# Kernel optimization log

Hardware: AMD Instinct MI355X
Metric: run time of the kernel (lower is better)

Reference implementation:

```python
import jax, jax.numpy as jnp
import numpy as np
import math

K = 8       # wavelet order (k)
C = 8       # channels (c)
ALPHA = 64  # retained Fourier modes
L = 0       # coarsest level
B = 32
N = 8192    # power of two


def setup_inputs() -> dict:
    key = jax.random.key(0)
    ks = jax.random.split(key, 14)
    ck = C * K
    scale = 1.0 / (ck * ck)  # matches torch: 1/(c*k)**2
    f32 = jnp.float32
    inp = {
        "x": jax.random.normal(ks[0], (B, N, C, K), dtype=f32),
        # SparseKernelFT1d weights (complex, stored as re/im): scale * rand
        "wA_re": scale * jax.random.uniform(ks[1], (ck, ck, ALPHA), dtype=f32),
        "wA_im": scale * jax.random.uniform(ks[2], (ck, ck, ALPHA), dtype=f32),
        "wB_re": scale * jax.random.uniform(ks[3], (ck, ck, ALPHA), dtype=f32),
        "wB_im": scale * jax.random.uniform(ks[4], (ck, ck, ALPHA), dtype=f32),
        "wC_re": scale * jax.random.uniform(ks[5], (ck, ck, ALPHA), dtype=f32),
        "wC_im": scale * jax.random.uniform(ks[6], (ck, ck, ALPHA), dtype=f32),
        # T0 linear layer (k -> k)
        "T0_w": jax.random.normal(ks[7], (K, K), dtype=f32) / math.sqrt(K),
        "T0_b": 0.01 * jax.random.normal(ks[8], (K,), dtype=f32),
        # Legendre wavelet filter buffers: ec_* are [H0.T;H1.T] / [G0.T;G1.T] (2k,k),
        # rc_* are [H0;G0] / [H1;G1] (2k,k). Stand-ins: random orthonormal-ish matrices
        # scaled like wavelet filters (same math regardless of exact values).
        "ec_s": jax.random.normal(ks[9], (2 * K, K), dtype=f32) / math.sqrt(2 * K),
        "ec_d": jax.random.normal(ks[10], (2 * K, K), dtype=f32) / math.sqrt(2 * K),
        "rc_e": jax.random.normal(ks[11], (2 * K, K), dtype=f32) / math.sqrt(2 * K),
        "rc_o": jax.random.normal(ks[12], (2 * K, K), dtype=f32) / math.sqrt(2 * K),
    }
    return inp


def _sparse_ft(x, w_re, w_im):
    # x: [B, N, c, k] -> spectral mixing over first ALPHA rfft modes
    Bb, Nn, c, k = x.shape
    xv = x.reshape(Bb, Nn, c * k).transpose(0, 2, 1)   # [B, ck, N]
    xf = jnp.fft.rfft(xv)                               # [B, ck, N//2+1] complex
    l = min(ALPHA, Nn // 2 + 1)
    W = (w_re[:, :, :l] + 1j * w_im[:, :, :l]).astype(jnp.complex64)
    of = jnp.einsum('bix,iox->box', xf[:, :, :l], W)
    out_ft = jnp.zeros((Bb, c * k, Nn // 2 + 1), dtype=jnp.complex64).at[:, :, :l].set(of)
    xo = jnp.fft.irfft(out_ft, n=Nn)                    # [B, ck, N] real
    return xo.transpose(0, 2, 1).reshape(Bb, Nn, c, k)


def reference(x, wA_re, wA_im, wB_re, wB_im, wC_re, wC_im, T0_w, T0_b,
              ec_s, ec_d, rc_e, rc_o):
    Bb, Nn, c, k = x.shape
    ns = int(math.floor(math.log2(Nn)))
    Ud, Us = [], []
    # --- decomposition ---
    for _ in range(ns - L):
        xa = jnp.concatenate([x[:, ::2], x[:, 1::2]], axis=-1)  # [B, N/2, c, 2k]
        d = xa @ ec_d                                           # [B, N/2, c, k]
        s = xa @ ec_s
        Ud.append(_sparse_ft(d, wA_re, wA_im) + _sparse_ft(s, wB_re, wB_im))
        Us.append(_sparse_ft(d, wC_re, wC_im))
        x = s
    # --- coarsest-level linear ---
    x = x @ T0_w.T + T0_b
    # --- reconstruction (u_s is None branch) ---
    for i in range(ns - 1 - L, -1, -1):
        x = x + Us[i]
        xc = jnp.concatenate([x, Ud[i]], axis=-1)               # [B, n, c, 2k]
        x_e = xc @ rc_e
        x_o = xc @ rc_o
        Bc, Nc, cc, _ = xc.shape
        x = jnp.stack([x_e, x_o], axis=2).reshape(Bc, Nc * 2, cc, K)  # interleave even/odd
    return (x,) + tuple(Ud) + tuple(Us)
```

## Files before the change

### kernel.cpp

```cpp
#include <hip/hip_runtime.h>

#define BB 32
#define CKD 64
#define CC 8
#define KK 8
#define TT 64
#define FPW 132

__device__ const int D_FCB[14] = {0,8,12,14,15,16,17,18,19,20,21,22,23,24};
__device__ const int D_TB[14] = {0,64,96,112,120,124,126,127,128,129,130,131,132,133};
__device__ const int D_LS[14] = {0,64,128,192,256,320,384,417,434,443,448,451,453,454};
__device__ const int D_L[13]  = {64,64,64,64,64,64,33,17,9,5,3,2,1};
__device__ const int D_FTOF[13] = {0,524288,786432,917504,983040,1015808,1032192,
                                   1048576,1064960,1081344,1097728,1114112,1130496};

typedef __attribute__((ext_vector_type(4))) short s4v;
typedef __attribute__((ext_vector_type(8))) short s8v;
typedef __attribute__((ext_vector_type(4))) float f4v;

static __device__ __forceinline__ float4 ld4(const float* p){ return *(const float4*)p; }
static __device__ __forceinline__ size_t d_udo(int i){ return 33554432ull - (16777216u >> i); }
static __device__ __forceinline__ size_t d_uso(int i){ return 50329600ull - (16777216u >> i); }
static __device__ __forceinline__ size_t d_tof(int i){ return 128ull * (8192u - (8192u >> i)); }

static __device__ __forceinline__ unsigned short b16(float f) {
    unsigned u = __float_as_uint(f);
    u += 0x7FFFu + ((u >> 16) & 1u);
    return (unsigned short)(u >> 16);
}
static __device__ __forceinline__ float fb16(unsigned short h) {
    return __uint_as_float(((unsigned)h) << 16);
}

__global__ __launch_bounds__(256) void gen_T_k(unsigned short* __restrict__ Th,
                                               unsigned short* __restrict__ Tl) {
    int lvl = blockIdx.y;
    int nh = 4096 >> lvl;
    int idx = blockIdx.x * 256 + threadIdx.x;
    if (idx >= nh * 128) return;
    int t = idx >> 7, k = idx & 127, x = k >> 1;
    int l = nh / 2 + 1; if (l > 64) l = 64;
    float v = 0.f;
    if (x < l) {
        int r = (x * t) & (nh - 1);
        float th = 6.283185307179586f * ((float)r / (float)nh);
        float s, c; sincosf(th, &s, &c);
        v = (k & 1) ? s : c;
    }
    unsigned short hi = b16(v);
    unsigned short lo = b16(v - fb16(hi));
    size_t off = d_tof(lvl) + idx;
    Th[off] = hi; Tl[off] = lo;
}

__global__ __launch_bounds__(256) void gen_Tf_k(unsigned short* __restrict__ Tfh,
                                                unsigned short* __restrict__ Tfl) {
    int lvl = blockIdx.y;
    int nh = 4096 >> lvl;
    int nhp = nh < 128 ? 128 : nh;
    int idx = blockIdx.x * 256 + threadIdx.x;
    if (idx >= 128 * nhp) return;
    int tb = 31 - __clz(nhp);
    int m = idx >> tb, t = idx & (nhp - 1);
    int x = m >> 1;
    int l = nh / 2 + 1; if (l > 64) l = 64;
    float v = 0.f;
    if (x < l && t < nh) {
        int r = (x * t) & (nh - 1);
        float th = 6.283185307179586f * ((float)r / (float)nh);
        float s, c; sincosf(th, &s, &c);
        v = (m & 1) ? -s : c;
    }
    unsigned short hi = b16(v);
    unsigned short lo = b16(v - fb16(hi));
    size_t off = (size_t)D_FTOF[lvl] + idx;
    Tfh[off] = hi; Tfl[off] = lo;
}

__global__ __launch_bounds__(256) void decomp_k(const float* __restrict__ xin,
        const float* __restrict__ ecd, const float* __restrict__ ecs,
        float* __restrict__ dslot, float* __restrict__ sslot, int nh) {
    int idx = blockIdx.x * 256 + threadIdx.x;
    if (idx >= BB * nh * CC) return;
    int c = idx & 7;
    int t = (idx >> 3) % nh;
    int b = idx / (nh * CC);
    const float* p0 = xin + ((size_t)b * 2 * nh + 2 * t) * CKD + c * KK;
    float xa[16];
    float4 v;
    v = ld4(p0);      xa[0]=v.x; xa[1]=v.y; xa[2]=v.z; xa[3]=v.w;
    v = ld4(p0+4);    xa[4]=v.x; xa[5]=v.y; xa[6]=v.z; xa[7]=v.w;
    v = ld4(p0+64);   xa[8]=v.x; xa[9]=v.y; xa[10]=v.z; xa[11]=v.w;
    v = ld4(p0+68);   xa[12]=v.x; xa[13]=v.y; xa[14]=v.z; xa[15]=v.w;
    float dd[8], ss[8];
    #pragma unroll
    for (int m = 0; m < 8; m++) { dd[m] = 0.f; ss[m] = 0.f; }
    #pragma unroll
    for (int j = 0; j < 16; j++) {
        float xv = xa[j];
        #pragma unroll
        for (int m = 0; m < 8; m++) {
            dd[m] = fmaf(xv, ecd[j*8+m], dd[m]);
            ss[m] = fmaf(xv, ecs[j*8+m], ss[m]);
        }
    }
    size_t ob = ((size_t)b * nh + t) * CKD + c * KK;
    *(float4*)(dslot+ob)   = make_float4(dd[0],dd[1],dd[2],dd[3]);
    *(float4*)(dslot+ob+4) = make_float4(dd[4],dd[5],dd[6],dd[7]);
    *(float4*)(sslot+ob)   = make_float4(ss[0],ss[1],ss[2],ss[3]);
    *(float4*)(sslot+ob+4) = make_float4(ss[4],ss[5],ss[6],ss[7]);
}

__global__ __launch_bounds__(256) void fft_fwd_mfma_k(const float* __restrict__ outbuf,
        const unsigned short* __restrict__ Tfh, const unsigned short* __restrict__ Tfl,
        float* __restrict__ xfpf) {
    __shared__ unsigned vp[64*FPW];
    int slot = blockIdx.x;
    int lvl = 0;
    while (lvl < 12 && slot >= D_FCB[lvl+1]) lvl++;
    int nh = 4096 >> lvl;
    int nhp = nh < 128 ? 128 : nh;
    int t0s = (slot - D_FCB[lvl]) * 512;
    int t1s = t0s + 512; if (t1s > nhp) t1s = nhp;
    int b = blockIdx.y, z = blockIdx.z;
    const float* V = outbuf + (z ? d_uso(lvl) : d_udo(lvl)) + (size_t)b * nh * CKD;
    const unsigned short* TH = Tfh + D_FTOF[lvl];
    const unsigned short* TL = Tfl + D_FTOF[lvl];
    int tid = threadIdx.x;
    int w = tid >> 6, lane = tid & 63;
    int col = lane & 15, khi = lane >> 4;
    int mt0 = (w & 1) * 4, nt0 = (w >> 1) * 2;
    f4v acc[4][2];
    #pragma unroll
    for (int m = 0; m < 4; m++)
        #pragma unroll
        for (int n = 0; n < 2; n++) acc[m][n] = (f4v){0.f,0.f,0.f,0.f};
    int rrow[2], rswz[2];
    #pragma unroll
    for (int n = 0; n < 2; n++) {
        rrow[n] = (nt0 + n)*16 + col;
        rswz[n] = ((rrow[n] >> 3) & 7) << 2;
    }
    for (int tc = t0s; tc < t1s; tc += 128) {
        __syncthreads();
        #pragma unroll
        for (int q = 0; q < 8; q++) {
            int fi = tid + 256*q;
            int t = tc + (fi >> 4);
            int i4 = (fi & 15) * 4;
            float4 v = make_float4(0.f,0.f,0.f,0.f);
            if (t < nh) v = ld4(V + (size_t)t*CKD + i4);
            int tl_ = t - tc;
            const float* pv = &v.x;
            #pragma unroll
            for (int j = 0; j < 4; j++) {
                int row = i4 + j;
                float f = pv[j];
                unsigned u = __float_as_uint(f);
                unsigned hi = u & 0xFFFF0000u;
                float r = f - __uint_as_float(hi);
                unsigned lo = __float_as_uint(r) & 0xFFFF0000u;
                int cw = tl_ ^ (((row >> 3) & 7) << 2);
                vp[row*FPW + cw] = (hi >> 16) | lo;
            }
        }
        __syncthreads();
        #pragma unroll
        for (int kk = 0; kk < 4; kk++) {
            int tg = tc + kk*32 + khi*8;
            s8v ah[4], al[4];
            #pragma unroll
            for (int m = 0; m < 4; m++) {
                int row = (mt0 + m)*16 + col;
                ah[m] = *(const s8v*)(TH + (size_t)row*nhp + tg);
                al[m] = *(const s8v*)(TL + (size_t)row*nhp + tg);
            }
            int cb = kk*32 + khi*8;
            #pragma unroll
            for (int n = 0; n < 2; n++) {
                const unsigned* pr = vp + rrow[n]*FPW;
                uint4 w0 = *(const uint4*)(pr + (cb ^ rswz[n]));
                uint4 w1 = *(const uint4*)(pr + ((cb + 4) ^ rswz[n]));
                s8v bh, bl;
                const unsigned* pw = &w0.x;
                #pragma unroll
                for (int j = 0; j < 4; j++) {
                    bh[j] = (short)(pw[j] & 0xFFFFu);
                    bl[j] = (short)(pw[j] >> 16);
                }
                pw = &w1.x;
                #pragma unroll
                for (int j = 0; j < 4; j++) {
                    bh[4+j] = (short)(pw[j] & 0xFFFFu);
                    bl[4+j] = (short)(pw[j] >> 16);
                }
                #pragma unroll
                for (int m = 0; m < 4; m++) {
                    acc[m][n] = __builtin_amdgcn_mfma_f32_16x16x32_bf16(ah[m], bh, acc[m][n], 0,0,0);
                    acc[m][n] = __builtin_amdgcn_mfma_f32_16x16x32_bf16(ah[m], bl, acc[m][n], 0,0,0);
                    acc[m][n] = __builtin_amdgcn_mfma_f32_16x16x32_bf16(al[m], bh, acc[m][n], 0,0,0);
                }
            }
        }
    }
    float* P = xfpf + ((size_t)slot*64 + (size_t)b*2 + z) * 8192;
    #pragma unroll
    for (int m = 0; m < 4; m++) {
        int m0 = (mt0 + m)*16 + khi*4;
        #pragma unroll
        for (int n = 0; n < 2; n++) {
            int ic = (nt0 + n)*16 + col;
            #pragma unroll
            for (int r = 0; r < 4; r++)
                P[(size_t)(m0 + r)*64 + ic] = acc[m][n][r];
        }
    }
}

__global__ __launch_bounds__(256) void reduce_fwd_k(const float* __restrict__ xfpf,
        float2* __restrict__ xf_all) {
    int lvl = blockIdx.y;
    int e = blockIdx.x * 256 + threadIdx.x;
    int j = e & 4095;
    int bz = e >> 12;
    int x = j >> 6, i = j & 63;
    int c0 = D_FCB[lvl], c1 = D_FCB[lvl+1];
    float re = 0.f, im = 0.f;
    for (int c = c0; c < c1; c++) {
        size_t base = ((size_t)c*64 + bz) * 8192;
        re += xfpf[base + (size_t)(2*x)*64 + i];
        im += xfpf[base + (size_t)(2*x+1)*64 + i];
    }
    xf_all[(size_t)lvl*262144 + (size_t)bz*4096 + j] = make_float2(re, im);
}

__global__ __launch_bounds__(256) void mix_all_k(const float2* __restrict__ xf_all,
        const float* __restrict__ wAr, const float* __restrict__ wAi,
        const float* __restrict__ wBr, const float* __restrict__ wBi,
        const float* __restrict__ wCr, const float* __restrict__ wCi,
        unsigned short* __restrict__ ofh, unsigned short* __restrict__ ofl) {
    int lvl = 0;
    while (lvl < 12 && (int)blockIdx.x >= D_LS[lvl+1]) lvl++;
    int x = blockIdx.x - D_LS[lvl];
    int nh = 4096 >> lvl;
    const float2* xfL = xf_all + (size_t)lvl*262144;
    int tid = threadIdx.x;
    int o = tid & 63, wq = tid >> 6;
    __shared__ float2 sxd[BB*CKD];
    __shared__ float2 sxs[BB*CKD];
    __shared__ float  swt[6][16*CKD];
    for (int q = tid; q < BB*CKD; q += 256) {
        int b = q >> 6, i = q & 63;
        sxd[q] = xfL[((size_t)b*2 + 0)*4096 + x*64 + i];
        sxs[q] = xfL[((size_t)b*2 + 1)*4096 + x*64 + i];
    }
    float2 aud[8], aus[8];
    #pragma unroll
    for (int j=0;j<8;j++){ aud[j]=make_float2(0.f,0.f); aus[j]=make_float2(0.f,0.f); }
    for (int ic = 0; ic < 4; ic++) {
        __syncthreads();
        for (int q = tid; q < 16*CKD; q += 256) {
            int ii = q >> 6, oo = q & 63;
            size_t a = ((size_t)(ic*16+ii)*64 + oo)*64 + x;
            swt[0][q] = wAr[a]; swt[1][q] = wAi[a];
            swt[2][q] = wBr[a]; swt[3][q] = wBi[a];
            swt[4][q] = wCr[a]; swt[5][q] = wCi[a];
        }
        __syncthreads();
        #pragma unroll 4
        for (int ii = 0; ii < 16; ii++) {
            float ar = swt[0][ii*64+o], ai_ = swt[1][ii*64+o];
            float br = swt[2][ii*64+o], bi_ = swt[3][ii*64+o];
            float cr = swt[4][ii*64+o], ci_ = swt[5][ii*64+o];
            int i = ic*16 + ii;
            #pragma unroll
            for (int j = 0; j < 8; j++) {
                float2 xd = sxd[(wq*8+j)*64 + i];
                float2 xs = sxs[(wq*8+j)*64 + i];
                aud[j].x += xd.x*ar - xd.y*ai_ + xs.x*br - xs.y*bi_;
                aud[j].y += xd.x*ai_ + xd.y*ar + xs.x*bi_ + xs.y*br;
                aus[j].x += xd.x*cr - xd.y*ci_;
                aus[j].y += xd.x*ci_ + xd.y*cr;
            }
        }
    }
    float w = (x == 0 || 2*x == nh) ? 1.f : 2.f;
    float sc = w / (float)nh;
    int k0 = 2*x;
    #pragma unroll
    for (int j = 0; j < 8; j++) {
        int b = wq*8 + j;
        {
            size_t base = (((size_t)lvl*32 + b)*2 + 0)*8192;
            float A = sc*aud[j].x, Bn = -sc*aud[j].y;
            unsigned short ha = b16(A),  hb = b16(Bn);
            unsigned short la = b16(A - fb16(ha)), lb = b16(Bn - fb16(hb));
            ofh[base + (size_t)k0*64 + o]     = ha;
            ofh[base + (size_t)(k0+1)*64 + o] = hb;
            ofl[base + (size_t)k0*64 + o]     = la;
            ofl[base + (size_t)(k0+1)*64 + o] = lb;
        }
        {
            size_t base = (((size_t)lvl*32 + b)*2 + 1)*8192;
            float A = sc*aus[j].x, Bn = -sc*aus[j].y;
            unsigned short ha = b16(A),  hb = b16(Bn);
            unsigned short la = b16(A - fb16(ha)), lb = b16(Bn - fb16(hb));
            ofh[base + (size_t)k0*64 + o]     = ha;
            ofh[base + (size_t)(k0+1)*64 + o] = hb;
            ofl[base + (size_t)k0*64 + o]     = la;
            ofl[base + (size_t)(k0+1)*64 + o] = lb;
        }
    }
}

__global__ __launch_bounds__(256) void fft_inv_mfma_k(
        const unsigned short* __restrict__ ofh, const unsigned short* __restrict__ ofl,
        const unsigned short* __restrict__ Th,  const unsigned short* __restrict__ Tl,
        float* __restrict__ outbuf) {
    __shared__ unsigned short gh[64*132];
    __shared__ unsigned short gl[64*132];
    int lvl = 0;
    while (lvl < 12 && (int)blockIdx.x >= D_TB[lvl+1]) lvl++;
    int g = blockIdx.x - D_TB[lvl];
    int nh = 4096 >> lvl;
    int tbase = g * 64;
    int b = blockIdx.y, z = blockIdx.z;
    const unsigned short* Gh = ofh + (((size_t)lvl*32 + b)*2 + z)*8192;
    const unsigned short* Gl = ofl + (((size_t)lvl*32 + b)*2 + z)*8192;
    int tid = threadIdx.x;
    #pragma unroll
    for (int q = 0; q < 4; q++) {
        int fi = tid + 256*q;
        int k = fi & 127, oct = fi >> 7;
        uint4 vh = *(const uint4*)(Gh + (size_t)k*64 + oct*8);
        uint4 vl = *(const uint4*)(Gl + (size_t)k*64 + oct*8);
        const unsigned* ph = &vh.x;
        const unsigned* pl = &vl.x;
        #pragma unroll
        for (int i = 0; i < 8; i++) {
            unsigned wd = ph[i>>1];
            gh[(oct*8+i)*132 + k] = (i&1) ? (unsigned short)(wd>>16) : (unsigned short)(wd&0xFFFF);
            wd = pl[i>>1];
            gl[(oct*8+i)*132 + k] = (i&1) ? (unsigned short)(wd>>16) : (unsigned short)(wd&0xFFFF);
        }
    }
    __syncthreads();
    int w = tid >> 6;
    int lane = tid & 63;
    int tb = tbase + w*16;
    if (tb >= nh) return;
    int trow = lane & 15, khi = lane >> 4;
    int tA = tb + trow; if (tA >= nh) tA = nh - 1;
    const unsigned short* THp = Th + d_tof(lvl) + (size_t)tA*128 + khi*8;
    const unsigned short* TLp = Tl + d_tof(lvl) + (size_t)tA*128 + khi*8;
    f4v acc[4];
    #pragma unroll
    for (int n = 0; n < 4; n++) acc[n] = (f4v){0.f,0.f,0.f,0.f};
    #pragma unroll
    for (int kk = 0; kk < 4; kk++) {
        s8v ah = *(const s8v*)(THp + kk*32);
        s8v al = *(const s8v*)(TLp + kk*32);
        #pragma unroll
        for (int n = 0; n < 4; n++) {
            int off = (n*16 + trow)*132 + kk*32 + khi*8;
            s4v b0 = *(const s4v*)(gh + off);
            s4v b1 = *(const s4v*)(gh + off + 4);
            s4v c0 = *(const s4v*)(gl + off);
            s4v c1 = *(const s4v*)(gl + off + 4);
            s8v bh = __builtin_shufflevector(b0, b1, 0,1,2,3,4,5,6,7);
            s8v bl = __builtin_shufflevector(c0, c1, 0,1,2,3,4,5,6,7);
            acc[n] = __builtin_amdgcn_mfma_f32_16x16x32_bf16(ah, bh, acc[n], 0, 0, 0);
            acc[n] = __builtin_amdgcn_mfma_f32_16x16x32_bf16(ah, bl, acc[n], 0, 0, 0);
            acc[n] = __builtin_amdgcn_mfma_f32_16x16x32_bf16(al, bh, acc[n], 0, 0, 0);
        }
    }
    float* U = outbuf + (z ? d_uso(lvl) : d_udo(lvl)) + (size_t)b * nh * CKD;
    int thi4 = (lane >> 4) * 4;
    #pragma unroll
    for (int n = 0; n < 4; n++) {
        #pragma unroll
        for (int r = 0; r < 4; r++) {
            int t = tb + thi4 + r;
            if (t < nh) U[(size_t)t*64 + n*16 + trow] = acc[n][r];
        }
    }
}

__global__ __launch_bounds__(256) void t0_k(const float* __restrict__ xin,
        const float* __restrict__ w, const float* __restrict__ bias,
        float* __restrict__ xout) {
    int idx = blockIdx.x*256 + threadIdx.x;
    if (idx >= BB*CKD) return;
    int m = idx & 7, c = (idx >> 3) & 7, b = idx >> 6;
    const float* xr = xin + (size_t)b*CKD + c*KK;
    float acc = bias[m];
    #pragma unroll
    for (int j = 0; j < 8; j++) acc = fmaf(xr[j], w[m*8+j], acc);
    xout[idx] = acc;
}

__global__ __launch_bounds__(256) void recon_k(const float* __restrict__ xin,
        const float* __restrict__ us, const float* __restrict__ ud,
        const float* __restrict__ rce, const float* __restrict__ rco,
        float* __restrict__ xout, int nh) {
    int idx = blockIdx.x*256 + threadIdx.x;
    if (idx >= BB*nh*CC) return;
    int c = idx & 7;
    int t = (idx >> 3) % nh;
    int b = idx / (nh*CC);
    size_t base = ((size_t)b*nh + t)*CKD + c*KK;
    float xc[16];
    float4 a0 = ld4(xin+base), a1 = ld4(xin+base+4);
    float4 u0 = ld4(us+base),  u1 = ld4(us+base+4);
    float4 d0 = ld4(ud+base),  d1 = ld4(ud+base+4);
    xc[0]=a0.x+u0.x; xc[1]=a0.y+u0.y; xc[2]=a0.z+u0.z; xc[3]=a0.w+u0.w;
    xc[4]=a1.x+u1.x; xc[5]=a1.y+u1.y; xc[6]=a1.z+u1.z; xc[7]=a1.w+u1.w;
    xc[8]=d0.x;  xc[9]=d0.y;  xc[10]=d0.z; xc[11]=d0.w;
    xc[12]=d1.x; xc[13]=d1.y; xc[14]=d1.z; xc[15]=d1.w;
    float e[8], o2[8];
    #pragma unroll
    for (int m = 0; m < 8; m++) { e[m] = 0.f; o2[m] = 0.f; }
    #pragma unroll
    for (int j = 0; j < 16; j++) {
        float xv = xc[j];
        #pragma unroll
        for (int m = 0; m < 8; m++) {
            e[m]  = fmaf(xv, rce[j*8+m], e[m]);
            o2[m] = fmaf(xv, rco[j*8+m], o2[m]);
        }
    }
    size_t ob = ((size_t)b*2*nh + 2*t)*CKD + c*KK;
    *(float4*)(xout+ob)      = make_float4(e[0],e[1],e[2],e[3]);
    *(float4*)(xout+ob+4)    = make_float4(e[4],e[5],e[6],e[7]);
    *(float4*)(xout+ob+64)   = make_float4(o2[0],o2[1],o2[2],o2[3]);
    *(float4*)(xout+ob+68)   = make_float4(o2[4],o2[5],o2[6],o2[7]);
}

extern "C" void kernel_launch(void* const* d_in, const int* in_sizes, int n_in,
                              void* d_out, int out_size, void* d_ws, size_t ws_size,
                              hipStream_t stream) {
    const float* x   = (const float*)d_in[0];
    const float* wAr = (const float*)d_in[1];
    const float* wAi = (const float*)d_in[2];
    const float* wBr = (const float*)d_in[3];
    const float* wBi = (const float*)d_in[4];
    const float* wCr = (const float*)d_in[5];
    const float* wCi = (const float*)d_in[6];
    const float* T0w = (const float*)d_in[7];
    const float* T0b = (const float*)d_in[8];
    const float* ecs = (const float*)d_in[9];
    const float* ecd = (const float*)d_in[10];
    const float* rce = (const float*)d_in[11];
    const float* rco = (const float*)d_in[12];
    float* out = (float*)d_out;
    float* wsf = (float*)d_ws;

    size_t p = 0;
    float2* xf_all = (float2*)(wsf + p); p += 6815744;
    unsigned short* ofh = (unsigned short*)(wsf + p); p += 3407872;
    unsigned short* ofl = (unsigned short*)(wsf + p); p += 3407872;
    unsigned short* Th  = (unsigned short*)(wsf + p); p += 528384;
    unsigned short* Tl  = (unsigned short*)(wsf + p); p += 528384;
    unsigned short* Tfh = (unsigned short*)(wsf + p); p += 573440;
    unsigned short* Tfl = (unsigned short*)(wsf + p); p += 573440;
    float*  xt0  = wsf + p; p += 2048;
    float*  rb0  = wsf + p; p += 4194304;
    float*  rb1  = wsf + p; p += 8388608;
    float*  xfpf = wsf + p; p += 12582912;
    (void)ws_size; (void)in_sizes; (void)n_in; (void)out_size;

    size_t udo[13], uso[13];
    for (int i = 0; i < 13; i++) {
        udo[i] = 33554432ull - (16777216u >> i);
        uso[i] = 50329600ull - (16777216u >> i);
    }

    gen_T_k<<<dim3(2048, 13), 256, 0, stream>>>(Th, Tl);
    gen_Tf_k<<<dim3(2048, 13), 256, 0, stream>>>(Tfh, Tfl);

    for (int i = 0; i < 13; i++) {
        int nh = 4096 >> i;
        const float* xin_l = (i == 0) ? x : (out + uso[i-1]);
        int tot = BB * nh * CC;
        decomp_k<<<(tot + 255)/256, 256, 0, stream>>>(xin_l, ecd, ecs, out + udo[i], out + uso[i], nh);
    }
    t0_k<<<(BB*CKD + 255)/256, 256, 0, stream>>>(out + uso[12], T0w, T0b, xt0);

    fft_fwd_mfma_k<<<dim3(24, BB, 2), 256, 0, stream>>>(out, Tfh, Tfl, xfpf);
    reduce_fwd_k<<<dim3(1024, 13), 256, 0, stream>>>(xfpf, xf_all);
    mix_all_k<<<454, 256, 0, stream>>>(xf_all, wAr, wAi, wBr, wBi, wCr, wCi, ofh, ofl);
    fft_inv_mfma_k<<<dim3(133, BB, 2), 256, 0, stream>>>(ofh, ofl, Th, Tl, out);

    const float* rin = xt0;
    for (int i = 12; i >= 0; i--) {
        int nh = 4096 >> i;
        float* ro = (i == 0) ? out : ((i & 1) ? rb1 : rb0);
        int tot = BB * nh * CC;
        recon_k<<<(tot + 255)/256, 256, 0, stream>>>(rin, out + uso[i], out + udo[i], rce, rco, ro, nh);
        rin = ro;
    }
}
```

Measured before the change: 508.2 us.

## Split forward DFT into finer time slices and pre-swizzle twiddles into MFMA layout

Each forward-DFT block now handles a single 128-sample time chunk instead of looping over up to 512 samples. This raises the grid from 24 to 70 slots per batch and channel set, to improve occupancy and latency hiding. The forward twiddle table is generated directly in the MFMA A-fragment order, so each lane loads a contiguous 16-byte vector instead of strided rows. In exchange there are many more partial results for reduce_fwd_k to sum, and the partial buffer grows by about three times, adding memory traffic.

```diff
diff --git a/kernel.cpp b/kernel.cpp
--- a/kernel.cpp
+++ b/kernel.cpp
@@ -7,7 +7,7 @@
 #define TT 64
 #define FPW 132
 
-__device__ const int D_FCB[14] = {0,8,12,14,15,16,17,18,19,20,21,22,23,24};
+__device__ const int D_FCB[14] = {0,32,48,56,60,62,63,64,65,66,67,68,69,70};
 __device__ const int D_TB[14] = {0,64,96,112,120,124,126,127,128,129,130,131,132,133};
 __device__ const int D_LS[14] = {0,64,128,192,256,320,384,417,434,443,448,451,453,454};
 __device__ const int D_L[13]  = {64,64,64,64,64,64,33,17,9,5,3,2,1};
@@ -60,16 +60,20 @@
     int nhp = nh < 128 ? 128 : nh;
     int idx = blockIdx.x * 256 + threadIdx.x;
     if (idx >= 128 * nhp) return;
-    int tb = 31 - __clz(nhp);
-    int m = idx >> tb, t = idx & (nhp - 1);
-    int x = m >> 1;
+    int j = idx & 7;
+    int lane = (idx >> 3) & 63;
+    int mt = (idx >> 9) & 7;
+    int kb = idx >> 12;
+    int row = mt*16 + (lane & 15);
+    int t = kb*32 + (lane >> 4)*8 + j;
+    int x = row >> 1;
     int l = nh / 2 + 1; if (l > 64) l = 64;
     float v = 0.f;
     if (x < l && t < nh) {
         int r = (x * t) & (nh - 1);
         float th = 6.283185307179586f * ((float)r / (float)nh);
         float s, c; sincosf(th, &s, &c);
-        v = (m & 1) ? -s : c;
+        v = (row & 1) ? -s : c;
     }
     unsigned short hi = b16(v);
     unsigned short lo = b16(v - fb16(hi));
@@ -119,87 +123,83 @@
     int lvl = 0;
     while (lvl < 12 && slot >= D_FCB[lvl+1]) lvl++;
     int nh = 4096 >> lvl;
-    int nhp = nh < 128 ? 128 : nh;
-    int t0s = (slot - D_FCB[lvl]) * 512;
-    int t1s = t0s + 512; if (t1s > nhp) t1s = nhp;
+    int t0s = (slot - D_FCB[lvl]) * 128;
     int b = blockIdx.y, z = blockIdx.z;
     const float* V = outbuf + (z ? d_uso(lvl) : d_udo(lvl)) + (size_t)b * nh * CKD;
-    const unsigned short* TH = Tfh + D_FTOF[lvl];
-    const unsigned short* TL = Tfl + D_FTOF[lvl];
+    const unsigned short* THb = Tfh + D_FTOF[lvl];
+    const unsigned short* TLb = Tfl + D_FTOF[lvl];
     int tid = threadIdx.x;
     int w = tid >> 6, lane = tid & 63;
     int col = lane & 15, khi = lane >> 4;
     int mt0 = (w & 1) * 4, nt0 = (w >> 1) * 2;
-    f4v acc[4][2];
-    #pragma unroll
-    for (int m = 0; m < 4; m++)
-        #pragma unroll
-        for (int n = 0; n < 2; n++) acc[m][n] = (f4v){0.f,0.f,0.f,0.f};
+    #pragma unroll
+    for (int q = 0; q < 8; q++) {
+        int fi = tid + 256*q;
+        int tl_ = fi >> 4;
+        int t = t0s + tl_;
+        int i4 = (fi & 15) * 4;
+        float4 v = make_float4(0.f,0.f,0.f,0.f);
+        if (t < nh) v = ld4(V + (size_t)t*CKD + i4);
+        const float* pv = &v.x;
+        #pragma unroll
+        for (int j = 0; j < 4; j++) {
+            int row = i4 + j;
+            float f = pv[j];
+            unsigned u = __float_as_uint(f);
+            unsigned hi = u & 0xFFFF0000u;
+            float r = f - __uint_as_float(hi);
+            unsigned lo = __float_as_uint(r) & 0xFFFF0000u;
+            int cw = tl_ ^ (((row >> 3) & 7) << 2);
+            vp[row*FPW + cw] = (hi >> 16) | lo;
+        }
+    }
+    __syncthreads();
     int rrow[2], rswz[2];
     #pragma unroll
     for (int n = 0; n < 2; n++) {
         rrow[n] = (nt0 + n)*16 + col;
         rswz[n] = ((rrow[n] >> 3) & 7) << 2;
     }
-    for (int tc = t0s; tc < t1s; tc += 128) {
-        __syncthreads();
-        #pragma unroll
-        for (int q = 0; q < 8; q++) {
-            int fi = tid + 256*q;
-            int t = tc + (fi >> 4);
-            int i4 = (fi & 15) * 4;
-            float4 v = make_float4(0.f,0.f,0.f,0.f);
-            if (t < nh) v = ld4(V + (size_t)t*CKD + i4);
-            int tl_ = t - tc;
-            const float* pv = &v.x;
+    f4v acc[4][2];
+    #pragma unroll
+    for (int m = 0; m < 4; m++)
+        #pragma unroll
+        for (int n = 0; n < 2; n++) acc[m][n] = (f4v){0.f,0.f,0.f,0.f};
+    int kb0 = (slot - D_FCB[lvl]) * 4;
+    #pragma unroll
+    for (int kk = 0; kk < 4; kk++) {
+        int kb = kb0 + kk;
+        s8v ah[4], al[4];
+        #pragma unroll
+        for (int m = 0; m < 4; m++) {
+            size_t fo = (((size_t)kb*8 + (mt0 + m))*64 + lane)*8;
+            ah[m] = *(const s8v*)(THb + fo);
+            al[m] = *(const s8v*)(TLb + fo);
+        }
+        int cb = kk*32 + khi*8;
+        #pragma unroll
+        for (int n = 0; n < 2; n++) {
+            const unsigned* pr = vp + rrow[n]*FPW;
+            uint4 w0 = *(const uint4*)(pr + (cb ^ rswz[n]));
+            uint4 w1 = *(const uint4*)(pr + ((cb + 4) ^ rswz[n]));
+            s8v bh, bl;
+            const unsigned* pw = &w0.x;
             #pragma unroll
             for (int j = 0; j < 4; j++) {
-                int row = i4 + j;
-                float f = pv[j];
-                unsigned u = __float_as_uint(f);
-                unsigned hi = u & 0xFFFF0000u;
-                float r = f - __uint_as_float(hi);
-                unsigned lo = __float_as_uint(r) & 0xFFFF0000u;
-                int cw = tl_ ^ (((row >> 3) & 7) << 2);
-                vp[row*FPW + cw] = (hi >> 16) | lo;
+                bh[j] = (short)(pw[j] & 0xFFFFu);
+                bl[j] = (short)(pw[j] >> 16);
             }
-        }
-        __syncthreads();
-        #pragma unroll
-        for (int kk = 0; kk < 4; kk++) {
-            int tg = tc + kk*32 + khi*8;
-            s8v ah[4], al[4];
+            pw = &w1.x;
+            #pragma unroll
+            for (int j = 0; j < 4; j++) {
+                bh[4+j] = (short)(pw[j] & 0xFFFFu);
+                bl[4+j] = (short)(pw[j] >> 16);
+            }
             #pragma unroll
             for (int m = 0; m < 4; m++) {
-                int row = (mt0 + m)*16 + col;
-                ah[m] = *(const s8v*)(TH + (size_t)row*nhp + tg);
-                al[m] = *(const s8v*)(TL + (size_t)row*nhp + tg);
-            }
-            int cb = kk*32 + khi*8;
-            #pragma unroll
-            for (int n = 0; n < 2; n++) {
-                const unsigned* pr = vp + rrow[n]*FPW;
-                uint4 w0 = *(const uint4*)(pr + (cb ^ rswz[n]));
-                uint4 w1 = *(const uint4*)(pr + ((cb + 4) ^ rswz[n]));
-                s8v bh, bl;
-                const unsigned* pw = &w0.x;
-                #pragma unroll
-                for (int j = 0; j < 4; j++) {
-                    bh[j] = (short)(pw[j] & 0xFFFFu);
-                    bl[j] = (short)(pw[j] >> 16);
-                }
-                pw = &w1.x;
-                #pragma unroll
-                for (int j = 0; j < 4; j++) {
-                    bh[4+j] = (short)(pw[j] & 0xFFFFu);
-                    bl[4+j] = (short)(pw[j] >> 16);
-                }
-                #pragma unroll
-                for (int m = 0; m < 4; m++) {
-                    acc[m][n] = __builtin_amdgcn_mfma_f32_16x16x32_bf16(ah[m], bh, acc[m][n], 0,0,0);
-                    acc[m][n] = __builtin_amdgcn_mfma_f32_16x16x32_bf16(ah[m], bl, acc[m][n], 0,0,0);
-                    acc[m][n] = __builtin_amdgcn_mfma_f32_16x16x32_bf16(al[m], bh, acc[m][n], 0,0,0);
-                }
+                acc[m][n] = __builtin_amdgcn_mfma_f32_16x16x32_bf16(ah[m], bh, acc[m][n], 0,0,0);
+                acc[m][n] = __builtin_amdgcn_mfma_f32_16x16x32_bf16(ah[m], bl, acc[m][n], 0,0,0);
+                acc[m][n] = __builtin_amdgcn_mfma_f32_16x16x32_bf16(al[m], bh, acc[m][n], 0,0,0);
             }
         }
     }
@@ -466,7 +466,7 @@
     float*  xt0  = wsf + p; p += 2048;
     float*  rb0  = wsf + p; p += 4194304;
     float*  rb1  = wsf + p; p += 8388608;
-    float*  xfpf = wsf + p; p += 12582912;
+    float*  xfpf = wsf + p; p += 36700160;
     (void)ws_size; (void)in_sizes; (void)n_in; (void)out_size;
 
     size_t udo[13], uso[13];
@@ -486,7 +486,7 @@
     }
     t0_k<<<(BB*CKD + 255)/256, 256, 0, stream>>>(out + uso[12], T0w, T0b, xt0);
 
-    fft_fwd_mfma_k<<<dim3(24, BB, 2), 256, 0, stream>>>(out, Tfh, Tfl, xfpf);
+    fft_fwd_mfma_k<<<dim3(70, BB, 2), 256, 0, stream>>>(out, Tfh, Tfl, xfpf);
     reduce_fwd_k<<<dim3(1024, 13), 256, 0, stream>>>(xfpf, xf_all);
     mix_all_k<<<454, 256, 0, stream>>>(xf_all, wAr, wAi, wBr, wBi, wCr, wCi, ofh, ofl);
     fft_inv_mfma_k<<<dim3(133, BB, 2), 256, 0, stream>>>(ofh, ofl, Th, Tl, out);
```

New measurement: 492.9 us. -3.0%, faster.
